# Optimization experiments

Measured on AMD Instinct MI355X. Metric: run time of the kernel, lower is better.

## Reference

```python
import jax, jax.numpy as jnp
import numpy as np

B, QH, QW = 16, 64, 64
KH, KW = 64, 64
H, D, DK, K, S = 8, 256, 32, 4, 1


def setup_inputs() -> dict:
    key = jax.random.key(0)
    ks = jax.random.split(key, 16)
    def lin(i, din, dout, wscale=1.0):
        w = jax.random.normal(ks[i], (din, dout), jnp.float32) * (wscale / np.sqrt(din))
        b = jax.random.normal(ks[i + 1], (dout,), jnp.float32) * 0.02
        return w, b
    Wq, bq = lin(0, D, D)
    Wb, bb = lin(2, D, D)
    Wk, bk = lin(4, D, D)
    Woff, boff = lin(6, D, 2 * H * K * S, wscale=0.1)  # small offsets keep samples near ref point
    WA, bA = lin(8, D, H * K * S)
    Wm, bm = lin(10, D, D)
    return dict(
        query=jax.random.normal(ks[12], (B, QH, QW, D), jnp.float32),
        keys=jax.random.normal(ks[13], (B, KH, KW, D), jnp.float32),
        ref_point=jax.random.uniform(ks[14], (B, QH, QW, 2), jnp.float32),
        src_query=jax.random.normal(ks[15], (B, QH, QW, D), jnp.float32),
        Wq=Wq, bq=bq, Wb=Wb, bb=bb, Wk=Wk, bk=bk,
        Woff=Woff, boff=boff, WA=WA, bA=bA, Wm=Wm, bm=bm)


def _bilinear_zeros(img, px, py):
    # img [N, Hs, Ws, C]; px, py pixel coords [N, K, QH, QW]
    # Matches torch F.grid_sample(mode='bilinear', padding_mode='zeros'):
    # each out-of-bounds corner contributes zero.
    N, Hs, Ws, _ = img.shape
    x0 = jnp.floor(px); y0 = jnp.floor(py)
    wx1 = px - x0; wy1 = py - y0
    n = jnp.arange(N)[:, None, None, None]
    def corner(xf, yf, w):
        xi = xf.astype(jnp.int32); yi = yf.astype(jnp.int32)
        valid = (xi >= 0) & (xi < Ws) & (yi >= 0) & (yi < Hs)
        v = img[n, jnp.clip(yi, 0, Hs - 1), jnp.clip(xi, 0, Ws - 1)]
        return v * (w * valid)[..., None]
    return (corner(x0, y0, (1 - wx1) * (1 - wy1)) + corner(x0 + 1, y0, wx1 * (1 - wy1))
            + corner(x0, y0 + 1, (1 - wx1) * wy1) + corner(x0 + 1, y0 + 1, wx1 * wy1))


def reference(query, keys, ref_point, src_query, Wq, bq, Wb, bb, Wk, bk,
              Woff, boff, WA, bA, Wm, bm):
    _ = query @ Wq + bq  # q_proj output is computed but unused in the original forward
    sq = src_query @ Wb + bb
    off = (sq @ Woff + boff).reshape(B, QH, QW, H, S, K, 2)
    off = off.transpose(0, 3, 4, 5, 1, 2, 6).reshape(B * H, S, K, QH, QW, 2)
    A = jax.nn.softmax((sq @ WA + bA).reshape(B, QH, QW, H, S * K), axis=-1)
    A = A.transpose(0, 3, 1, 2, 4).reshape(B * H, QH, QW, S, K)
    # k_proj on the (single-scale) key feature map -> per-head maps [B*H, KH, KW, DK]
    kf = (keys @ Wk + bk).reshape(B, KH, KW, H, DK).transpose(0, 3, 1, 2, 4).reshape(B * H, KH, KW, DK)
    # restore_scale then torch .repeat(h,1,1,1): flat index n -> batch n % B (faithful to original)
    rr = ref_point * jnp.array([KW - 1, KH - 1], jnp.float32)
    rr = jnp.tile(rr, (H, 1, 1, 1))  # [B*H, QH, QW, 2]
    samples = []
    for l in range(S):
        pts = rr[:, None] + off[:, l]                 # [B*H, K, QH, QW, 2]
        vgx = 2.0 * pts[..., 0] / max(KW - 1, 1) - 1.0
        vgy = 2.0 * pts[..., 1] / max(KH - 1, 1) - 1.0
        px = ((vgx + 1.0) * KW - 1.0) / 2.0           # grid_sample align_corners=False unnormalize
        py = ((vgy + 1.0) * KH - 1.0) / 2.0
        samples.append(_bilinear_zeros(kf, px, py))   # [B*H, K, QH, QW, DK]
    samp = jnp.stack(samples, axis=1)                 # [B*H, S, K, QH, QW, DK]
    feat = jnp.einsum('nskhwd,nhwsk->nhwd', samp, A)  # weighted sum over scales*points
    feat = feat.reshape(B, H, QH, QW, DK).transpose(0, 2, 3, 1, 4).reshape(B, QH, QW, D)
    return feat @ Wm + bm
```

## Files before the change

### kernel.cpp

```cpp
#include <hip/hip_runtime.h>
#include <hip/hip_bf16.h>

using bf16 = __hip_bfloat16;
typedef short bf16x8 __attribute__((ext_vector_type(8)));
typedef float f32x4 __attribute__((ext_vector_type(4)));
typedef unsigned int u32x4 __attribute__((ext_vector_type(4)));

#define DD 256
#define MTOT 65536

static __device__ __forceinline__ short f2bs(float f) {
    bf16 h = __float2bfloat16(f);
    return *reinterpret_cast<short*>(&h);
}
static __device__ __forceinline__ float bs2f(short s) {
    unsigned u = (unsigned)(unsigned short)s << 16;
    return __uint_as_float(u);
}

static __device__ __forceinline__ void gll16(const void* g, void* l) {
    __builtin_amdgcn_global_load_lds(
        (const __attribute__((address_space(1))) unsigned int*)g,
        (__attribute__((address_space(3))) unsigned int*)l, 16, 0, 0);
}

static __device__ __forceinline__ int swz_idx(int n, int k) {
    return n * 256 + ((((k >> 3) ^ (n & 7)) << 3) | (k & 7));
}

__global__ __launch_bounds__(256) void k_setup(
    const float* __restrict__ Wk, const float* __restrict__ Wm,
    bf16* __restrict__ WkT, bf16* __restrict__ WmT,
    const float* __restrict__ Wb, const float* __restrict__ bb,
    const float* __restrict__ Woff, const float* __restrict__ boff,
    const float* __restrict__ WA, const float* __restrict__ bA,
    bf16* __restrict__ WCt, float* __restrict__ bc)
{
    __shared__ float colw[256];
    __shared__ float red[256];
    int bid = blockIdx.x, t = threadIdx.x;
    if (bid < 512) {
        int idx = bid * 256 + t;
        int which = idx >> 16, e = idx & 65535;
        int i = e >> 8, j = e & 255;
        const float* src = which == 0 ? Wk : Wm;
        bf16*        dst = which == 0 ? WkT : WmT;
        dst[swz_idx(j, i)] = __float2bfloat16(src[e]);
        return;
    }
    int j = bid - 512;
    float cw = (j < 64) ? Woff[t * 64 + j] : WA[t * 32 + (j - 64)];
    colw[t] = cw;
    red[t] = bb[t] * cw;
    __syncthreads();
    float v = 0.f;
    const float* wbrow = Wb + (size_t)t * 256;
#pragma unroll 8
    for (int i = 0; i < 256; ++i) v += wbrow[i] * colw[i];
    WCt[swz_idx(j, t)] = __float2bfloat16(v);
    for (int s = 128; s > 0; s >>= 1) {
        __syncthreads();
        if (t < s) red[t] += red[t + s];
    }
    if (t == 0) bc[j] = red[0] + ((j < 64) ? boff[j] : bA[j - 64]);
}

template <int NTW, int NCOLS, bool AF32>
static __device__ __forceinline__ void gemm_lds2(
    const void* __restrict__ Av, const bf16* __restrict__ BTswz,
    bf16* __restrict__ Bs, char* __restrict__ As,
    int row0, int tid, f32x4 (&acc)[2][NTW])
{
    const int wave = tid >> 6, lane = tid & 63;
    const int rg = wave >> 1, cg = wave & 1;
    const int rsub = lane & 15, kg = lane >> 4;
    constexpr int SB = NCOLS / 32;
    constexpr int SA = AF32 ? 4 : 2;
    constexpr int ABYTES = AF32 ? 16384 : 8192;

    auto stageB = [&](int s) {
#pragma unroll
        for (int i = 0; i < SB; ++i) {
            int cc = wave * SB + i;
            int i16 = cc * 64 + lane;
            int n = i16 >> 3, lg = i16 & 7;
            gll16(BTswz + (size_t)n * 256 + s * 64 + lg * 8, (char*)Bs + (size_t)i16 * 16);
        }
    };
    auto stageA = [&](int s, int buf) {
#pragma unroll
        for (int i = 0; i < SA; ++i) {
            if constexpr (AF32) {
                int cc = wave * 4 + i;
                int row = cc * 4 + (lane >> 4);
                int g = (lane & 15) ^ (row & 15);
                gll16((const float*)Av + (size_t)(row0 + row) * DD + s * 64 + g * 4,
                      As + (size_t)buf * ABYTES + cc * 1024 + lane * 16);
            } else {
                int cc = wave * 2 + i;
                int row = cc * 8 + (lane >> 3);
                int g = (lane & 7) ^ (row & 7);
                gll16((const bf16*)Av + (size_t)(row0 + row) * DD + s * 64 + g * 8,
                      As + (size_t)buf * ABYTES + cc * 1024 + lane * 16);
            }
        }
    };

    stageA(0, 0);
    int cur = 0;
#pragma unroll
    for (int s = 0; s < 4; ++s) {
        stageB(s);
        if (s < 3) {
            stageA(s + 1, cur ^ 1);
            asm volatile("s_waitcnt vmcnt(%0)" :: "i"(SA) : "memory");
        } else {
            asm volatile("s_waitcnt vmcnt(0)" ::: "memory");
        }
        __builtin_amdgcn_s_barrier();
#pragma unroll
        for (int kkl = 0; kkl < 2; ++kkl) {
            bf16x8 afr[2];
#pragma unroll
            for (int st = 0; st < 2; ++st) {
                int row = rg * 32 + st * 16 + rsub;
                if constexpr (AF32) {
                    const char* base = As + cur * ABYTES + row * 256;
                    int G0 = kkl * 8 + kg * 2;
                    f32x4 v0 = *(const f32x4*)(base + ((G0 ^ (row & 15)) << 4));
                    f32x4 v1 = *(const f32x4*)(base + (((G0 + 1) ^ (row & 15)) << 4));
                    bf16x8 a;
#pragma unroll
                    for (int e = 0; e < 4; ++e) { a[e] = f2bs(v0[e]); a[e + 4] = f2bs(v1[e]); }
                    afr[st] = a;
                } else {
                    const char* base = As + cur * ABYTES + row * 128;
                    int g = kkl * 4 + kg;
                    afr[st] = *(const bf16x8*)(base + ((g ^ (row & 7)) << 4));
                }
            }
            int lg = kkl * 4 + kg;
#pragma unroll
            for (int nt = 0; nt < NTW; ++nt) {
                int n = cg * (NTW * 16) + nt * 16 + rsub;
                bf16x8 b = *(const bf16x8*)((const char*)Bs + (size_t)n * 128 + ((lg ^ (n & 7)) << 4));
                acc[0][nt] = __builtin_amdgcn_mfma_f32_16x16x32_bf16(afr[0], b, acc[0][nt], 0, 0, 0);
                acc[1][nt] = __builtin_amdgcn_mfma_f32_16x16x32_bf16(afr[1], b, acc[1][nt], 0, 0, 0);
            }
        }
        asm volatile("s_waitcnt lgkmcnt(0)" ::: "memory");
        __builtin_amdgcn_s_barrier();
        cur ^= 1;
    }
}

__global__ __launch_bounds__(256) void k_offA(
    const float* __restrict__ src, const bf16* __restrict__ WCt, const float* __restrict__ bc,
    float* __restrict__ off_ws, float* __restrict__ A_ws)
{
    __shared__ __align__(16) bf16 Bs[96 * 64];
    __shared__ __align__(16) char As[2 * 16384];
    int tid = threadIdx.x, lane = tid & 63, wave = tid >> 6;
    int row0 = blockIdx.x * 64;
    f32x4 acc[2][3] = {};
    gemm_lds2<3, 96, true>(src, WCt, Bs, As, row0, tid, acc);
    int col = lane & 15;
    int jbase = (wave & 1) * 48;
    int rb = row0 + (wave >> 1) * 32 + ((lane >> 4) << 2);
#pragma unroll
    for (int mt = 0; mt < 2; ++mt) {
#pragma unroll
        for (int nt = 0; nt < 3; ++nt) {
            int j = jbase + nt * 16 + col;
            if (j < 64) {
                float bias = bc[j];
#pragma unroll
                for (int r = 0; r < 4; ++r) {
                    int m = rb + mt * 16 + r;
                    off_ws[(size_t)m * 64 + j] = acc[mt][nt][r] + bias;
                }
            } else {
                int ac = j - 64;
                float bias = bc[j];
#pragma unroll
                for (int r = 0; r < 4; ++r) {
                    int m = rb + mt * 16 + r;
                    float v  = acc[mt][nt][r] + bias;
                    float mx = fmaxf(v, __shfl_xor(v, 1));
                    mx       = fmaxf(mx, __shfl_xor(mx, 2));
                    float e  = __expf(v - mx);
                    float su = e + __shfl_xor(e, 1);
                    su      += __shfl_xor(su, 2);
                    A_ws[(size_t)m * 32 + ac] = e / su;
                }
            }
        }
    }
}

__global__ __launch_bounds__(256) void k_gemm_kf(
    const float* __restrict__ keys, const bf16* __restrict__ WkT,
    const float* __restrict__ bk, bf16* __restrict__ kf)
{
    __shared__ __align__(16) bf16 Bs[256 * 64];
    __shared__ __align__(16) char As[2 * 16384];
    int tid = threadIdx.x, lane = tid & 63, wave = tid >> 6;
    int row0 = blockIdx.x * 64;
    f32x4 acc[2][8] = {};
    gemm_lds2<8, 256, true>(keys, WkT, Bs, As, row0, tid, acc);
    int col = lane & 15;
    int jbase = (wave & 1) * 128;
    int rb = row0 + (wave >> 1) * 32 + ((lane >> 4) << 2);
#pragma unroll
    for (int mt = 0; mt < 2; ++mt)
#pragma unroll
        for (int nt = 0; nt < 8; ++nt) {
            int j = jbase + nt * 16 + col;
            float bias = bk[j];
#pragma unroll
            for (int r = 0; r < 4; ++r) {
                int m = rb + mt * 16 + r;
                size_t dst = (((size_t)(m >> 12) * 8 + (j >> 5)) * 4096 + (m & 4095)) * 32 + (j & 31);
                kf[dst] = __float2bfloat16(acc[mt][nt][r] + bias);
            }
        }
}

__global__ __launch_bounds__(256) void k_sample(
    const float* __restrict__ ref_point, const float* __restrict__ off_ws,
    const float* __restrict__ A_ws, const bf16* __restrict__ kf,
    bf16* __restrict__ feat)
{
    int bid = blockIdx.x;
    int xcd = bid & 7, within = bid >> 3;
    int b = xcd * 2 + (within >> 9);
    int pixblk = within & 511;
    int t  = threadIdx.x;
    int q  = t >> 5;
    int h  = (t >> 2) & 7;
    int cg = t & 3;
    int m  = (b << 12) + pixblk * 8 + q;
    int pix = m & 4095;
    int rbatch = (b * 8 + h) & 15;
    const float* rp = ref_point + ((size_t)rbatch * 4096 + pix) * 2;
    float rx = rp[0] * 63.0f;
    float ry = rp[1] * 63.0f;
    const bf16* kfh = kf + ((size_t)(b * 8 + h) * 4096) * 32 + cg * 8;
    f32x4 o0 = *(const f32x4*)(off_ws + (size_t)m * 64 + h * 8);
    f32x4 o1 = *(const f32x4*)(off_ws + (size_t)m * 64 + h * 8 + 4);
    f32x4 av = *(const f32x4*)(A_ws  + (size_t)m * 32 + h * 4);

    float w00[4], w01[4], w10[4], w11[4];
    const bf16 *p00[4], *p01[4], *p10[4], *p11[4];
#pragma unroll
    for (int k = 0; k < 4; ++k) {
        float ox = (k < 2) ? o0[2 * k] : o1[2 * k - 4];
        float oy = (k < 2) ? o0[2 * k + 1] : o1[2 * k - 3];
        float a  = av[k];
        float px = (rx + ox) * (64.0f / 63.0f) - 0.5f;
        float py = (ry + oy) * (64.0f / 63.0f) - 0.5f;
        float x0 = floorf(px), y0 = floorf(py);
        float wx1 = px - x0, wy1 = py - y0;
        int xi = (int)x0, yi = (int)y0;
        float ax0 = (1.f - wx1) * ((xi     >= 0 && xi     < 64) ? 1.f : 0.f);
        float ax1 = wx1         * ((xi + 1 >= 0 && xi + 1 < 64) ? 1.f : 0.f);
        float ay0 = (1.f - wy1) * ((yi     >= 0 && yi     < 64) ? a : 0.f);
        float ay1 = wy1         * ((yi + 1 >= 0 && yi + 1 < 64) ? a : 0.f);
        int xc0 = min(max(xi, 0), 63),      xc1 = min(max(xi + 1, 0), 63);
        int yc0 = min(max(yi, 0), 63) * 64, yc1 = min(max(yi + 1, 0), 63) * 64;
        w00[k] = ax0 * ay0; w01[k] = ax1 * ay0; w10[k] = ax0 * ay1; w11[k] = ax1 * ay1;
        p00[k] = kfh + (yc0 + xc0) * 32;
        p01[k] = kfh + (yc0 + xc1) * 32;
        p10[k] = kfh + (yc1 + xc0) * 32;
        p11[k] = kfh + (yc1 + xc1) * 32;
    }
    bf16x8 v00[4], v01[4], v10[4], v11[4];
#pragma unroll
    for (int k = 0; k < 4; ++k) {
        v00[k] = *(const bf16x8*)p00[k];
        v01[k] = *(const bf16x8*)p01[k];
        v10[k] = *(const bf16x8*)p10[k];
        v11[k] = *(const bf16x8*)p11[k];
    }
    float acc[8] = {};
#pragma unroll
    for (int k = 0; k < 4; ++k) {
        u32x4 u00 = __builtin_bit_cast(u32x4, v00[k]);
        u32x4 u01 = __builtin_bit_cast(u32x4, v01[k]);
        u32x4 u10 = __builtin_bit_cast(u32x4, v10[k]);
        u32x4 u11 = __builtin_bit_cast(u32x4, v11[k]);
#pragma unroll
        for (int d = 0; d < 4; ++d) {
            acc[2 * d]     += w00[k] * __uint_as_float(u00[d] << 16)
                            + w01[k] * __uint_as_float(u01[d] << 16)
                            + w10[k] * __uint_as_float(u10[d] << 16)
                            + w11[k] * __uint_as_float(u11[d] << 16);
            acc[2 * d + 1] += w00[k] * __uint_as_float(u00[d] & 0xffff0000u)
                            + w01[k] * __uint_as_float(u01[d] & 0xffff0000u)
                            + w10[k] * __uint_as_float(u10[d] & 0xffff0000u)
                            + w11[k] * __uint_as_float(u11[d] & 0xffff0000u);
        }
    }
    bf16x8 o;
#pragma unroll
    for (int e = 0; e < 8; ++e) o[e] = f2bs(acc[e]);
    *(bf16x8*)(feat + (size_t)m * DD + h * 32 + cg * 8) = o;
}

__global__ __launch_bounds__(256) void k_gemm_out(
    const bf16* __restrict__ feat, const bf16* __restrict__ WmT,
    const float* __restrict__ bm, float* __restrict__ out)
{
    __shared__ __align__(16) bf16 Bs[256 * 64];
    __shared__ __align__(16) char As[2 * 8192];
    int tid = threadIdx.x, lane = tid & 63, wave = tid >> 6;
    int row0 = blockIdx.x * 64;
    f32x4 acc[2][8] = {};
    gemm_lds2<8, 256, false>(feat, WmT, Bs, As, row0, tid, acc);
    int col = lane & 15;
    int jbase = (wave & 1) * 128;
    int rb = row0 + (wave >> 1) * 32 + ((lane >> 4) << 2);
#pragma unroll
    for (int mt = 0; mt < 2; ++mt)
#pragma unroll
        for (int nt = 0; nt < 8; ++nt) {
            int j = jbase + nt * 16 + col;
            float bias = bm[j];
#pragma unroll
            for (int r = 0; r < 4; ++r)
                out[(size_t)(rb + mt * 16 + r) * DD + j] =
                    acc[mt][nt][r] + bias;
        }
}

extern "C" void kernel_launch(void* const* d_in, const int* in_sizes, int n_in,
                              void* d_out, int out_size, void* d_ws, size_t ws_size,
                              hipStream_t stream)
{
    (void)in_sizes; (void)n_in; (void)out_size; (void)ws_size;
    const float* keys = (const float*)d_in[1];
    const float* refp = (const float*)d_in[2];
    const float* srcq = (const float*)d_in[3];
    const float* Wb   = (const float*)d_in[6];
    const float* bb   = (const float*)d_in[7];
    const float* Wk   = (const float*)d_in[8];
    const float* bk   = (const float*)d_in[9];
    const float* Woff = (const float*)d_in[10];
    const float* boff = (const float*)d_in[11];
    const float* WA   = (const float*)d_in[12];
    const float* bA   = (const float*)d_in[13];
    const float* Wm   = (const float*)d_in[14];
    const float* bm   = (const float*)d_in[15];

    char* ws = (char*)d_ws;
    bf16*  WkT    = (bf16*)(ws + 0);
    bf16*  WmT    = (bf16*)(ws + 131072);
    bf16*  WCt    = (bf16*)(ws + 262144);
    float* bc     = (float*)(ws + 311296);
    bf16*  kf_ws  = (bf16*)(ws + 442368 + 33554432ull);
    bf16*  feat_ws= (bf16*)(ws + 442368 + 2ull * 33554432ull);
    float* off_ws = (float*)(ws + 442368 + 3ull * 33554432ull);
    float* A_ws   = (float*)(ws + 442368 + 3ull * 33554432ull + 16777216ull);

    float* out = (float*)d_out;

    k_setup    <<<608, 256, 0, stream>>>(Wk, Wm, WkT, WmT, Wb, bb, Woff, boff, WA, bA, WCt, bc);
    k_offA     <<<1024, 256, 0, stream>>>(srcq, WCt, bc, off_ws, A_ws);
    k_gemm_kf  <<<1024, 256, 0, stream>>>(keys, WkT, bk, kf_ws);
    k_sample   <<<8192, 256, 0, stream>>>(refp, off_ws, A_ws, kf_ws, feat_ws);
    k_gemm_out <<<1024, 256, 0, stream>>>(feat_ws, WmT, bm, out);
}
```

Baseline: 118.1 us.

## Stage fp32 A operand through registers as bf16, restructure sampling loop, split sample launch

The fp32-input GEMMs now load A tiles into registers, convert them to bf16, and write them to LDS. This halves the A LDS footprint and removes per-fragment conversions in the MFMA loop, but it costs register pressure and an extra vmcnt wait before each write. The sampling kernel interleaves the corner loads with their accumulation per point instead of issuing all 16 loads up front, which lowers register use but may expose load latency. The sample kernel is also launched as two halves, and sched barriers are added to the bf16 GEMM.

```diff
diff --git a/kernel.cpp b/kernel.cpp
--- a/kernel.cpp
+++ b/kernel.cpp
@@ -3,6 +3,7 @@
 
 using bf16 = __hip_bfloat16;
 typedef short bf16x8 __attribute__((ext_vector_type(8)));
+typedef short s16x4 __attribute__((ext_vector_type(4)));
 typedef float f32x4 __attribute__((ext_vector_type(4)));
 typedef unsigned int u32x4 __attribute__((ext_vector_type(4)));
 
@@ -12,10 +13,6 @@
 static __device__ __forceinline__ short f2bs(float f) {
     bf16 h = __float2bfloat16(f);
     return *reinterpret_cast<short*>(&h);
-}
-static __device__ __forceinline__ float bs2f(short s) {
-    unsigned u = (unsigned)(unsigned short)s << 16;
-    return __uint_as_float(u);
 }
 
 static __device__ __forceinline__ void gll16(const void* g, void* l) {
@@ -65,9 +62,9 @@
     if (t == 0) bc[j] = red[0] + ((j < 64) ? boff[j] : bA[j - 64]);
 }
 
-template <int NTW, int NCOLS, bool AF32>
-static __device__ __forceinline__ void gemm_lds2(
-    const void* __restrict__ Av, const bf16* __restrict__ BTswz,
+template <int NTW, int NCOLS>
+static __device__ __forceinline__ void gemm_lds3(
+    const float* __restrict__ Av, const bf16* __restrict__ BTswz,
     bf16* __restrict__ Bs, char* __restrict__ As,
     int row0, int tid, f32x4 (&acc)[2][NTW])
 {
@@ -75,9 +72,29 @@
     const int rg = wave >> 1, cg = wave & 1;
     const int rsub = lane & 15, kg = lane >> 4;
     constexpr int SB = NCOLS / 32;
-    constexpr int SA = AF32 ? 4 : 2;
-    constexpr int ABYTES = AF32 ? 16384 : 8192;
-
+    const int arow_l = lane >> 4;
+    const int kb  = (lane & 15) * 4;
+    const int g_l = (lane & 15) >> 1;
+    const int sub = (lane & 15) & 1;
+
+    f32x4 areg[4];
+    auto loadA = [&](int s) {
+#pragma unroll
+        for (int c = 0; c < 4; ++c) {
+            int row = wave * 16 + c * 4 + arow_l;
+            areg[c] = *(const f32x4*)(Av + (size_t)(row0 + row) * DD + s * 64 + kb);
+        }
+    };
+    auto writeA = [&](int buf) {
+#pragma unroll
+        for (int c = 0; c < 4; ++c) {
+            int row = wave * 16 + c * 4 + arow_l;
+            s16x4 p;
+#pragma unroll
+            for (int e = 0; e < 4; ++e) p[e] = f2bs(areg[c][e]);
+            *(s16x4*)(As + buf * 8192 + row * 128 + ((g_l ^ (row & 7)) << 4) + sub * 8) = p;
+        }
+    };
     auto stageB = [&](int s) {
 #pragma unroll
         for (int i = 0; i < SB; ++i) {
@@ -87,22 +104,81 @@
             gll16(BTswz + (size_t)n * 256 + s * 64 + lg * 8, (char*)Bs + (size_t)i16 * 16);
         }
     };
+
+    loadA(0);
+    asm volatile("s_waitcnt vmcnt(0)" ::: "memory");
+    writeA(0);
+    int cur = 0;
+#pragma unroll
+    for (int s = 0; s < 4; ++s) {
+        stageB(s);
+        __builtin_amdgcn_sched_barrier(0);
+        if (s < 3) {
+            loadA(s + 1);
+            asm volatile("s_waitcnt vmcnt(4)" ::: "memory");
+        } else {
+            asm volatile("s_waitcnt vmcnt(0)" ::: "memory");
+        }
+        asm volatile("s_waitcnt lgkmcnt(0)" ::: "memory");
+        __builtin_amdgcn_s_barrier();
+#pragma unroll
+        for (int kkl = 0; kkl < 2; ++kkl) {
+            bf16x8 afr[2];
+#pragma unroll
+            for (int st = 0; st < 2; ++st) {
+                int row = rg * 32 + st * 16 + rsub;
+                int g = kkl * 4 + kg;
+                afr[st] = *(const bf16x8*)(As + cur * 8192 + row * 128 + ((g ^ (row & 7)) << 4));
+            }
+            int lg = kkl * 4 + kg;
+#pragma unroll
+            for (int nt = 0; nt < NTW; ++nt) {
+                int n = cg * (NTW * 16) + nt * 16 + rsub;
+                bf16x8 b = *(const bf16x8*)((const char*)Bs + (size_t)n * 128 + ((lg ^ (n & 7)) << 4));
+                acc[0][nt] = __builtin_amdgcn_mfma_f32_16x16x32_bf16(afr[0], b, acc[0][nt], 0, 0, 0);
+                acc[1][nt] = __builtin_amdgcn_mfma_f32_16x16x32_bf16(afr[1], b, acc[1][nt], 0, 0, 0);
+            }
+        }
+        if (s < 3) {
+            asm volatile("s_waitcnt vmcnt(0)" ::: "memory");
+            writeA(cur ^ 1);
+        }
+        asm volatile("s_waitcnt lgkmcnt(0)" ::: "memory");
+        __builtin_amdgcn_s_barrier();
+        cur ^= 1;
+    }
+}
+
+template <int NTW, int NCOLS>
+static __device__ __forceinline__ void gemm_lds2b(
+    const bf16* __restrict__ Av, const bf16* __restrict__ BTswz,
+    bf16* __restrict__ Bs, char* __restrict__ As,
+    int row0, int tid, f32x4 (&acc)[2][NTW])
+{
+    const int wave = tid >> 6, lane = tid & 63;
+    const int rg = wave >> 1, cg = wave & 1;
+    const int rsub = lane & 15, kg = lane >> 4;
+    constexpr int SB = NCOLS / 32;
+    constexpr int SA = 2;
+    constexpr int ABYTES = 8192;
+
+    auto stageB = [&](int s) {
+#pragma unroll
+        for (int i = 0; i < SB; ++i) {
+            int cc = wave * SB + i;
+            int i16 = cc * 64 + lane;
+            int n = i16 >> 3, lg = i16 & 7;
+            gll16(BTswz + (size_t)n * 256 + s * 64 + lg * 8, (char*)Bs + (size_t)i16 * 16);
+        }
+    };
     auto stageA = [&](int s, int buf) {
 #pragma unroll
         for (int i = 0; i < SA; ++i) {
-            if constexpr (AF32) {
-                int cc = wave * 4 + i;
-                int row = cc * 4 + (lane >> 4);
-                int g = (lane & 15) ^ (row & 15);
-                gll16((const float*)Av + (size_t)(row0 + row) * DD + s * 64 + g * 4,
-                      As + (size_t)buf * ABYTES + cc * 1024 + lane * 16);
-            } else {
-                int cc = wave * 2 + i;
-                int row = cc * 8 + (lane >> 3);
-                int g = (lane & 7) ^ (row & 7);
-                gll16((const bf16*)Av + (size_t)(row0 + row) * DD + s * 64 + g * 8,
-                      As + (size_t)buf * ABYTES + cc * 1024 + lane * 16);
-            }
+            int cc = wave * 2 + i;
+            int row = cc * 8 + (lane >> 3);
+            int g = (lane & 7) ^ (row & 7);
+            gll16(Av + (size_t)(row0 + row) * DD + s * 64 + g * 8,
+                  As + (size_t)buf * ABYTES + cc * 1024 + lane * 16);
         }
     };
 
@@ -111,6 +187,7 @@
 #pragma unroll
     for (int s = 0; s < 4; ++s) {
         stageB(s);
+        __builtin_amdgcn_sched_barrier(0);
         if (s < 3) {
             stageA(s + 1, cur ^ 1);
             asm volatile("s_waitcnt vmcnt(%0)" :: "i"(SA) : "memory");
@@ -124,20 +201,9 @@
 #pragma unroll
             for (int st = 0; st < 2; ++st) {
                 int row = rg * 32 + st * 16 + rsub;
-                if constexpr (AF32) {
-                    const char* base = As + cur * ABYTES + row * 256;
-                    int G0 = kkl * 8 + kg * 2;
-                    f32x4 v0 = *(const f32x4*)(base + ((G0 ^ (row & 15)) << 4));
-                    f32x4 v1 = *(const f32x4*)(base + (((G0 + 1) ^ (row & 15)) << 4));
-                    bf16x8 a;
-#pragma unroll
-                    for (int e = 0; e < 4; ++e) { a[e] = f2bs(v0[e]); a[e + 4] = f2bs(v1[e]); }
-                    afr[st] = a;
-                } else {
-                    const char* base = As + cur * ABYTES + row * 128;
-                    int g = kkl * 4 + kg;
-                    afr[st] = *(const bf16x8*)(base + ((g ^ (row & 7)) << 4));
-                }
+                const char* base = As + cur * ABYTES + row * 128;
+                int g = kkl * 4 + kg;
+                afr[st] = *(const bf16x8*)(base + ((g ^ (row & 7)) << 4));
             }
             int lg = kkl * 4 + kg;
 #pragma unroll
@@ -159,11 +225,11 @@
     float* __restrict__ off_ws, float* __restrict__ A_ws)
 {
     __shared__ __align__(16) bf16 Bs[96 * 64];
-    __shared__ __align__(16) char As[2 * 16384];
+    __shared__ __align__(16) char As[2 * 8192];
     int tid = threadIdx.x, lane = tid & 63, wave = tid >> 6;
     int row0 = blockIdx.x * 64;
     f32x4 acc[2][3] = {};
-    gemm_lds2<3, 96, true>(src, WCt, Bs, As, row0, tid, acc);
+    gemm_lds3<3, 96>(src, WCt, Bs, As, row0, tid, acc);
     int col = lane & 15;
     int jbase = (wave & 1) * 48;
     int rb = row0 + (wave >> 1) * 32 + ((lane >> 4) << 2);
@@ -203,11 +269,11 @@
     const float* __restrict__ bk, bf16* __restrict__ kf)
 {
     __shared__ __align__(16) bf16 Bs[256 * 64];
-    __shared__ __align__(16) char As[2 * 16384];
+    __shared__ __align__(16) char As[2 * 8192];
     int tid = threadIdx.x, lane = tid & 63, wave = tid >> 6;
     int row0 = blockIdx.x * 64;
     f32x4 acc[2][8] = {};
-    gemm_lds2<8, 256, true>(keys, WkT, Bs, As, row0, tid, acc);
+    gemm_lds3<8, 256>(keys, WkT, Bs, As, row0, tid, acc);
     int col = lane & 15;
     int jbase = (wave & 1) * 128;
     int rb = row0 + (wave >> 1) * 32 + ((lane >> 4) << 2);
@@ -229,9 +295,9 @@
 __global__ __launch_bounds__(256) void k_sample(
     const float* __restrict__ ref_point, const float* __restrict__ off_ws,
     const float* __restrict__ A_ws, const bf16* __restrict__ kf,
-    bf16* __restrict__ feat)
-{
-    int bid = blockIdx.x;
+    bf16* __restrict__ feat, int blk0)
+{
+    int bid = blockIdx.x + blk0;
     int xcd = bid & 7, within = bid >> 3;
     int b = xcd * 2 + (within >> 9);
     int pixblk = within & 511;
@@ -249,9 +315,7 @@
     f32x4 o0 = *(const f32x4*)(off_ws + (size_t)m * 64 + h * 8);
     f32x4 o1 = *(const f32x4*)(off_ws + (size_t)m * 64 + h * 8 + 4);
     f32x4 av = *(const f32x4*)(A_ws  + (size_t)m * 32 + h * 4);
-
-    float w00[4], w01[4], w10[4], w11[4];
-    const bf16 *p00[4], *p01[4], *p10[4], *p11[4];
+    float acc[8] = {};
 #pragma unroll
     for (int k = 0; k < 4; ++k) {
         float ox = (k < 2) ? o0[2 * k] : o1[2 * k - 4];
@@ -268,37 +332,25 @@
         float ay1 = wy1         * ((yi + 1 >= 0 && yi + 1 < 64) ? a : 0.f);
         int xc0 = min(max(xi, 0), 63),      xc1 = min(max(xi + 1, 0), 63);
         int yc0 = min(max(yi, 0), 63) * 64, yc1 = min(max(yi + 1, 0), 63) * 64;
-        w00[k] = ax0 * ay0; w01[k] = ax1 * ay0; w10[k] = ax0 * ay1; w11[k] = ax1 * ay1;
-        p00[k] = kfh + (yc0 + xc0) * 32;
-        p01[k] = kfh + (yc0 + xc1) * 32;
-        p10[k] = kfh + (yc1 + xc0) * 32;
-        p11[k] = kfh + (yc1 + xc1) * 32;
-    }
-    bf16x8 v00[4], v01[4], v10[4], v11[4];
-#pragma unroll
-    for (int k = 0; k < 4; ++k) {
-        v00[k] = *(const bf16x8*)p00[k];
-        v01[k] = *(const bf16x8*)p01[k];
-        v10[k] = *(const bf16x8*)p10[k];
-        v11[k] = *(const bf16x8*)p11[k];
-    }
-    float acc[8] = {};
-#pragma unroll
-    for (int k = 0; k < 4; ++k) {
-        u32x4 u00 = __builtin_bit_cast(u32x4, v00[k]);
-        u32x4 u01 = __builtin_bit_cast(u32x4, v01[k]);
-        u32x4 u10 = __builtin_bit_cast(u32x4, v10[k]);
-        u32x4 u11 = __builtin_bit_cast(u32x4, v11[k]);
+        float w00 = ax0 * ay0, w01 = ax1 * ay0, w10 = ax0 * ay1, w11 = ax1 * ay1;
+        bf16x8 v00 = *(const bf16x8*)(kfh + (yc0 + xc0) * 32);
+        bf16x8 v01 = *(const bf16x8*)(kfh + (yc0 + xc1) * 32);
+        bf16x8 v10 = *(const bf16x8*)(kfh + (yc1 + xc0) * 32);
+        bf16x8 v11 = *(const bf16x8*)(kfh + (yc1 + xc1) * 32);
+        u32x4 u00 = __builtin_bit_cast(u32x4, v00);
+        u32x4 u01 = __builtin_bit_cast(u32x4, v01);
+        u32x4 u10 = __builtin_bit_cast(u32x4, v10);
+        u32x4 u11 = __builtin_bit_cast(u32x4, v11);
 #pragma unroll
         for (int d = 0; d < 4; ++d) {
-            acc[2 * d]     += w00[k] * __uint_as_float(u00[d] << 16)
-                            + w01[k] * __uint_as_float(u01[d] << 16)
-                            + w10[k] * __uint_as_float(u10[d] << 16)
-                            + w11[k] * __uint_as_float(u11[d] << 16);
-            acc[2 * d + 1] += w00[k] * __uint_as_float(u00[d] & 0xffff0000u)
-                            + w01[k] * __uint_as_float(u01[d] & 0xffff0000u)
-                            + w10[k] * __uint_as_float(u10[d] & 0xffff0000u)
-                            + w11[k] * __uint_as_float(u11[d] & 0xffff0000u);
+            acc[2 * d]     += w00 * __uint_as_float(u00[d] << 16)
+                            + w01 * __uint_as_float(u01[d] << 16)
+                            + w10 * __uint_as_float(u10[d] << 16)
+                            + w11 * __uint_as_float(u11[d] << 16);
+            acc[2 * d + 1] += w00 * __uint_as_float(u00[d] & 0xffff0000u)
+                            + w01 * __uint_as_float(u01[d] & 0xffff0000u)
+                            + w10 * __uint_as_float(u10[d] & 0xffff0000u)
+                            + w11 * __uint_as_float(u11[d] & 0xffff0000u);
         }
     }
     bf16x8 o;
@@ -316,7 +368,7 @@
     int tid = threadIdx.x, lane = tid & 63, wave = tid >> 6;
     int row0 = blockIdx.x * 64;
     f32x4 acc[2][8] = {};
-    gemm_lds2<8, 256, false>(feat, WmT, Bs, As, row0, tid, acc);
+    gemm_lds2b<8, 256>(feat, WmT, Bs, As, row0, tid, acc);
     int col = lane & 15;
     int jbase = (wave & 1) * 128;
     int rb = row0 + (wave >> 1) * 32 + ((lane >> 4) << 2);
@@ -367,6 +419,7 @@
     k_setup    <<<608, 256, 0, stream>>>(Wk, Wm, WkT, WmT, Wb, bb, Woff, boff, WA, bA, WCt, bc);
     k_offA     <<<1024, 256, 0, stream>>>(srcq, WCt, bc, off_ws, A_ws);
     k_gemm_kf  <<<1024, 256, 0, stream>>>(keys, WkT, bk, kf_ws);
-    k_sample   <<<8192, 256, 0, stream>>>(refp, off_ws, A_ws, kf_ws, feat_ws);
+    k_sample   <<<4096, 256, 0, stream>>>(refp, off_ws, A_ws, kf_ws, feat_ws, 0);
+    k_sample   <<<4096, 256, 0, stream>>>(refp, off_ws, A_ws, kf_ws, feat_ws, 4096);
     k_gemm_out <<<1024, 256, 0, stream>>>(feat_ws, WmT, bm, out);
 }
```

New measurement: 119.0 us. About the same (+0.8%).
